# Kernel optimization log

Measured on AMD Instinct MI355X. Metric: run time of the kernel, lower is better.

Reference implementation:

```python
import jax, jax.numpy as jnp
import numpy as np

N_QUBITS = 14
W_MUL = (2.0 ** 0.5) * (5.0 ** -0.5)  # he_std = gain * 5**-0.5, lrmul = 1
TWO_PI = 2.0 * np.pi


def _rx(t):
    c = jnp.cos(t / 2); s = jnp.sin(t / 2)
    return jnp.stack([jnp.stack([c + 0j, -1j * s]), jnp.stack([-1j * s, c + 0j])])


def _ry(t):
    c = jnp.cos(t / 2); s = jnp.sin(t / 2)
    return jnp.stack([jnp.stack([c + 0j, -s + 0j]), jnp.stack([s + 0j, c + 0j])])


def _rz(t):
    e = jnp.exp(-0.5j * t); z = jnp.zeros_like(e)
    return jnp.stack([jnp.stack([e, z]), jnp.stack([z, jnp.conj(e)])])


def _apply_1q(state, gate, q):
    # state: (B,) + (2,)*n ; apply 2x2 gate on qubit q (axis q+1)
    ax = q + 1
    out = jnp.tensordot(gate, state, axes=([1], [ax]))  # new qubit axis at front
    return jnp.moveaxis(out, 0, ax)


_CNOT = jnp.array([[1, 0, 0, 0],
                   [0, 1, 0, 0],
                   [0, 0, 0, 1],
                   [0, 0, 1, 0]], dtype=jnp.complex64).reshape(2, 2, 2, 2)


def _apply_cnot(state, c, t):
    # _CNOT indices: [out_c, out_t, in_c, in_t]
    out = jnp.tensordot(_CNOT, state, axes=([2, 3], [c + 1, t + 1]))
    return jnp.moveaxis(out, (0, 1), (c + 1, t + 1))


def _rot_layer(state, params, gates):
    # per-qubit triple of rotations: params[3*i + j] for gate j on qubit i
    for i in range(N_QUBITS):
        for j, g in enumerate(gates):
            state = _apply_1q(state, g(params[3 * i + j]), i)
    return state


def _ring_of_cnot(state):
    for i in range(N_QUBITS):
        state = _apply_cnot(state, i, (i + 1) % N_QUBITS)
    return state


def _forward(x_real, x_imag, weight):
    n = N_QUBITS
    B = x_real.shape[0]
    psi = (x_real + 1j * x_imag).astype(jnp.complex64).reshape((B,) + (2,) * n)
    w = weight * W_MUL
    layers = [(_rx, _ry, _rz),  # XYZLayer
              (_ry, _rz, _ry),  # YZYLayer
              (_rz, _ry, _rx),  # ZYXLayer
              (_rx, _rz, _rx),  # XZXLayer
              (_ry, _rz, _ry)]  # YZYLayer
    for li, gates in enumerate(layers):
        psi = _rot_layer(psi, w[3 * n * li: 3 * n * (li + 1)], gates)
        if li < len(layers) - 1:
            psi = _ring_of_cnot(psi)
    Z = jnp.array([[1, 0], [0, -1]], dtype=jnp.complex64)
    zpsi = _apply_1q(psi, Z, 0)
    # <psi| Z_0 |psi> (original: conj(psi) row-vector @ (Z_0 psi) column-vector, take real)
    ev = jnp.sum(jnp.conj(psi) * zpsi, axis=tuple(range(1, n + 1))).real
    return ev.reshape(B, 1)  # matches torch (B,1,1).squeeze(-1)


def setup_inputs() -> dict:
    key = jax.random.key(0)
    k1, k2, k3 = jax.random.split(key, 3)
    B = 512
    dim = 2 ** N_QUBITS
    x_real = jax.random.normal(k1, (B, 1, dim), dtype=jnp.float32)
    x_imag = jax.random.normal(k2, (B, 1, dim), dtype=jnp.float32)
    weight = jax.random.uniform(k3, (15 * N_QUBITS,), dtype=jnp.float32) * TWO_PI
    return {"x_real": x_real, "x_imag": x_imag, "weight": weight}


def reference(x_real, x_imag, weight):
    return _forward(x_real, x_imag, weight)
```

## Files before the change

### kernel.cpp

```cpp
#include <hip/hip_runtime.h>
#include <hip/hip_bf16.h>

#define NQ   14
#define DIM  16384
#define BLK  1024
#define WMUL 0.6324555320336759f

typedef float v2f __attribute__((ext_vector_type(2)));

struct C2 { float x, y; };
__device__ inline C2 cmulc(C2 a, C2 b){ return C2{a.x*b.x - a.y*b.y, a.x*b.y + a.y*b.x}; }
__device__ inline C2 caddc(C2 a, C2 b){ return C2{a.x+b.x, a.y+b.y}; }
__device__ inline void mm2(const C2* a, const C2* b, C2* o) {
    o[0] = caddc(cmulc(a[0],b[0]), cmulc(a[1],b[2]));
    o[1] = caddc(cmulc(a[0],b[1]), cmulc(a[1],b[3]));
    o[2] = caddc(cmulc(a[2],b[0]), cmulc(a[3],b[2]));
    o[3] = caddc(cmulc(a[2],b[1]), cmulc(a[3],b[3]));
}
__device__ inline void build_gate(int ty, float t, C2* g) {
    float sn, cs;
    __sincosf(0.5f * t, &sn, &cs);
    if (ty == 0) {
        g[0] = C2{cs, 0.f}; g[1] = C2{0.f, -sn};
        g[2] = C2{0.f, -sn}; g[3] = C2{cs, 0.f};
    } else if (ty == 1) {
        g[0] = C2{cs, 0.f}; g[1] = C2{-sn, 0.f};
        g[2] = C2{sn, 0.f}; g[3] = C2{cs, 0.f};
    } else {
        g[0] = C2{cs, -sn}; g[1] = C2{0.f, 0.f};
        g[2] = C2{0.f, 0.f}; g[3] = C2{cs, sn};
    }
}
__device__ const int TYPES[5][3] = {
    {0,1,2},
    {1,2,1},
    {2,1,0},
    {0,2,0},
    {1,2,1},
};

__global__ void prep_kernel(const float* __restrict__ w, v2f* __restrict__ gg) {
    const int tid = threadIdx.x;
    if (tid < 5 * NQ) {
        const int li = tid / NQ, q = tid % NQ;
        C2 M[4], G[4], T[4];
        #pragma unroll
        for (int j = 0; j < 3; ++j) {
            float t = w[3 * NQ * li + 3 * q + j] * WMUL;
            build_gate(TYPES[li][j], t, G);
            if (j == 0) { M[0]=G[0]; M[1]=G[1]; M[2]=G[2]; M[3]=G[3]; }
            else { mm2(G, M, T); M[0]=T[0]; M[1]=T[1]; M[2]=T[2]; M[3]=T[3]; }
        }
        v2f* gb = &gg[tid * 8];
        #pragma unroll
        for (int k = 0; k < 4; ++k) {
            gb[k * 2 + 0] = v2f{ M[k].x, M[k].x};
            gb[k * 2 + 1] = v2f{-M[k].y, M[k].y};
        }
        if (tid == 4 * NQ + 0) {
            float* mm = (float*)&gg[5 * NQ * 8];
            mm[0] = M[0].x*M[0].x + M[0].y*M[0].y - (M[2].x*M[2].x + M[2].y*M[2].y);
            mm[1] = M[1].x*M[1].x + M[1].y*M[1].y - (M[3].x*M[3].x + M[3].y*M[3].y);
            mm[2] = (M[0].x*M[1].x + M[0].y*M[1].y) - (M[2].x*M[3].x + M[2].y*M[3].y);
            mm[3] = (M[0].x*M[1].y - M[0].y*M[1].x) - (M[2].x*M[3].y - M[2].y*M[3].x);
        }
    }
}

__device__ inline constexpr uint32_t slotf(uint32_t i){
    return i ^ (((i>>4) ^ (i>>8) ^ (i>>12)) & 15u);
}
template<int B> __device__ inline uint32_t ins0(uint32_t t){
    return ((t & ~((1u<<B)-1u)) << 1) | (t & ((1u<<B)-1u));
}
template<int B0,int B1,int B2> __device__ inline uint32_t expand3(uint32_t t){
    return ins0<B2>(ins0<B1>(ins0<B0>(t)));
}
template<int B0,int B1,int B2> __device__ inline constexpr uint32_t rmask3(int r){
    return ((r&1)?(1u<<B0):0u) | ((r&2)?(1u<<B1):0u) | ((r&4)?(1u<<B2):0u);
}

template<int J>
__device__ inline void rot8(v2f* v, const v2f* __restrict__ g){
    const v2f a00=g[0], b00=g[1], a01=g[2], b01=g[3];
    const v2f a10=g[4], b10=g[5], a11=g[6], b11=g[7];
    #pragma unroll
    for (int r = 0; r < 8; ++r){
        if (!(r & (1 << J))) {
            v2f x0 = v[r], x1 = v[r | (1 << J)];
            v2f s0 = x0.yx, s1 = x1.yx;
            v2f y0 = a00*x0 + b00*s0 + a01*x1 + b01*s1;
            v2f y1 = a10*x0 + b10*s0 + a11*x1 + b11*s1;
            v[r] = y0; v[r | (1<<J)] = y1;
        }
    }
}
template<int C, int T>
__device__ inline void cnot8(v2f* v){
    #pragma unroll
    for (int r = 0; r < 8; ++r){
        if ((r & (1 << C)) && !(r & (1 << T))) {
            v2f tt = v[r]; v[r] = v[r | (1 << T)]; v[r | (1 << T)] = tt;
        }
    }
}
template<int T>
__device__ inline void cnotSel(v2f* v, bool c){
    #pragma unroll
    for (int r = 0; r < 8; ++r){
        if (!(r & (1 << T))) {
            v2f lo = v[r], hi = v[r | (1 << T)];
            v[r]          = c ? hi : lo;
            v[r | (1<<T)] = c ? lo : hi;
        }
    }
}

__global__ __launch_bounds__(BLK) void qsim_kernel(
        const float* __restrict__ xr, const float* __restrict__ xi,
        const v2f* __restrict__ gg, float* __restrict__ out) {
    __shared__ v2f s[DIM];
    __shared__ float red[BLK / 64];

    const int b   = blockIdx.x;
    const uint32_t tid = threadIdx.x;

    const float* xrb = xr + (size_t)b * DIM;
    const float* xib = xi + (size_t)b * DIM;

    #define GMP(li, q) (&gg[((li) * NQ + (q)) * 8])

    #define PASS(B0, B1, B2, ...)                                                  \
        _Pragma("unroll 1")                                                        \
        for (uint32_t sl = 0; sl < 2; ++sl) {                                      \
            const uint32_t t  = tid + sl * BLK;                                    \
            const uint32_t sb = slotf(expand3<B0,B1,B2>(t));                       \
            v2f v[8];                                                              \
            _Pragma("unroll")                                                      \
            for (int r = 0; r < 8; ++r)                                            \
                v[r] = s[sb ^ slotf(rmask3<B0,B1,B2>(r))];                         \
            __VA_ARGS__                                                            \
            _Pragma("unroll")                                                      \
            for (int r = 0; r < 8; ++r)                                            \
                s[sb ^ slotf(rmask3<B0,B1,B2>(r))] = v[r];                         \
        }                                                                          \
        __syncthreads();

    float local = 0.f;

    #pragma unroll 1
    for (int li = 0; li < 4; ++li) {
        #pragma unroll 1
        for (uint32_t sl = 0; sl < 2; ++sl) {
            const uint32_t t = tid + sl * BLK;
            v2f v[8];
            if (li == 0) {
                #pragma unroll
                for (int r = 0; r < 8; ++r) {
                    uint32_t i = t | ((uint32_t)r << 11);
                    v[r] = v2f{xrb[i], xib[i]};
                }
            } else {
                const uint32_t sb = slotf(expand3<11,12,13>(t));
                #pragma unroll
                for (int r = 0; r < 8; ++r)
                    v[r] = s[sb ^ slotf(rmask3<11,12,13>(r))];
            }
            rot8<2>(v, GMP(li,0)); rot8<1>(v, GMP(li,1)); rot8<0>(v, GMP(li,2));
            cnot8<2,1>(v); cnot8<1,0>(v);
            const uint32_t sb = slotf(expand3<11,12,13>(t));
            #pragma unroll
            for (int r = 0; r < 8; ++r)
                s[sb ^ slotf(rmask3<11,12,13>(r))] = v[r];
        }
        __syncthreads();

        PASS(8,9,10,
            rot8<2>(v, GMP(li,3)); rot8<1>(v, GMP(li,4)); rot8<0>(v, GMP(li,5));
            cnotSel<2>(v, (t >> 8) & 1u);
            cnot8<2,1>(v); cnot8<1,0>(v);
        )
        PASS(5,6,7,
            rot8<2>(v, GMP(li,6)); rot8<1>(v, GMP(li,7)); rot8<0>(v, GMP(li,8));
            cnotSel<2>(v, (t >> 5) & 1u);
            cnot8<2,1>(v); cnot8<1,0>(v);
        )
        PASS(2,3,4,
            rot8<2>(v, GMP(li,9)); rot8<1>(v, GMP(li,10)); rot8<0>(v, GMP(li,11));
            cnotSel<2>(v, (t >> 2) & 1u);
            cnot8<2,1>(v); cnot8<1,0>(v);
        )
        #pragma unroll 1
        for (uint32_t sl = 0; sl < 2; ++sl) {
            const uint32_t t  = tid + sl * BLK;
            const uint32_t sb = slotf(expand3<0,1,13>(t));
            v2f v[8];
            #pragma unroll
            for (int r = 0; r < 8; ++r)
                v[r] = s[sb ^ slotf(rmask3<0,1,13>(r))];
            rot8<1>(v, GMP(li,12)); rot8<0>(v, GMP(li,13));
            cnotSel<1>(v, t & 1u);
            cnot8<1,0>(v);
            cnot8<0,2>(v);
            if (li < 3) {
                #pragma unroll
                for (int r = 0; r < 8; ++r)
                    s[sb ^ slotf(rmask3<0,1,13>(r))] = v[r];
            } else {
                const float* mm = (const float*)&gg[5 * NQ * 8];
                const float mA = mm[0], mB = mm[1], mP = mm[2], mQ = mm[3];
                #pragma unroll
                for (int r = 0; r < 4; ++r) {
                    v2f a0 = v[r], a1 = v[r | 4];
                    float n0 = a0.x*a0.x + a0.y*a0.y;
                    float n1 = a1.x*a1.x + a1.y*a1.y;
                    float u  = a0.x*a1.x + a0.y*a1.y;
                    float vv = a0.x*a1.y - a0.y*a1.x;
                    local += mA*n0 + mB*n1 + 2.f*(mP*u - mQ*vv);
                }
            }
        }
        if (li < 3) __syncthreads();
    }

    #pragma unroll
    for (int off = 32; off > 0; off >>= 1) local += __shfl_down(local, off);
    const int lane = tid & 63, wid = tid >> 6;
    if (lane == 0) red[wid] = local;
    __syncthreads();
    if (tid == 0) {
        float t = 0.f;
        #pragma unroll
        for (int k = 0; k < BLK / 64; ++k) t += red[k];
        out[b] = t;
    }
}

extern "C" void kernel_launch(void* const* d_in, const int* in_sizes, int n_in,
                              void* d_out, int out_size, void* d_ws, size_t ws_size,
                              hipStream_t stream) {
    const float* xr = (const float*)d_in[0];
    const float* xi = (const float*)d_in[1];
    const float* w  = (const float*)d_in[2];
    float* out = (float*)d_out;
    v2f* gg = (v2f*)d_ws;
    const int B = out_size;
    prep_kernel<<<1, 128, 0, stream>>>(w, gg);
    qsim_kernel<<<B, BLK, 0, stream>>>(xr, xi, gg, out);
}
```

Baseline: 109.6 us.

## Process both slots per thread in split real/imag packed-float layout

Replaces the per-slot sequential loop with a single pass where each thread holds both slots at once. Amplitudes are repacked as separate real and imaginary v2f vectors whose lanes are the two slots, so rotations become packed scalar-broadcast FMAs with no swizzle. Gate coefficients are now stored as plain floats. The intent is to improve packed-FMA use and expose more memory-level parallelism. The cost is doubled register pressure per thread at 1024-thread blocks, plus extra pack and unpack work around each shared-memory access.

```diff
diff --git a/kernel.cpp b/kernel.cpp
--- a/kernel.cpp
+++ b/kernel.cpp
@@ -39,7 +39,7 @@
     {1,2,1},
 };
 
-__global__ void prep_kernel(const float* __restrict__ w, v2f* __restrict__ gg) {
+__global__ void prep_kernel(const float* __restrict__ w, float* __restrict__ gg) {
     const int tid = threadIdx.x;
     if (tid < 5 * NQ) {
         const int li = tid / NQ, q = tid % NQ;
@@ -51,14 +51,11 @@
             if (j == 0) { M[0]=G[0]; M[1]=G[1]; M[2]=G[2]; M[3]=G[3]; }
             else { mm2(G, M, T); M[0]=T[0]; M[1]=T[1]; M[2]=T[2]; M[3]=T[3]; }
         }
-        v2f* gb = &gg[tid * 8];
+        float* gb = &gg[tid * 8];
         #pragma unroll
-        for (int k = 0; k < 4; ++k) {
-            gb[k * 2 + 0] = v2f{ M[k].x, M[k].x};
-            gb[k * 2 + 1] = v2f{-M[k].y, M[k].y};
-        }
+        for (int k = 0; k < 4; ++k) { gb[k*2] = M[k].x; gb[k*2+1] = M[k].y; }
         if (tid == 4 * NQ + 0) {
-            float* mm = (float*)&gg[5 * NQ * 8];
+            float* mm = &gg[5 * NQ * 8];
             mm[0] = M[0].x*M[0].x + M[0].y*M[0].y - (M[2].x*M[2].x + M[2].y*M[2].y);
             mm[1] = M[1].x*M[1].x + M[1].y*M[1].y - (M[3].x*M[3].x + M[3].y*M[3].y);
             mm[2] = (M[0].x*M[1].x + M[0].y*M[1].y) - (M[2].x*M[3].x + M[2].y*M[3].y);
@@ -70,10 +67,10 @@
 __device__ inline constexpr uint32_t slotf(uint32_t i){
     return i ^ (((i>>4) ^ (i>>8) ^ (i>>12)) & 15u);
 }
-template<int B> __device__ inline uint32_t ins0(uint32_t t){
+template<int B> __device__ inline constexpr uint32_t ins0(uint32_t t){
     return ((t & ~((1u<<B)-1u)) << 1) | (t & ((1u<<B)-1u));
 }
-template<int B0,int B1,int B2> __device__ inline uint32_t expand3(uint32_t t){
+template<int B0,int B1,int B2> __device__ inline constexpr uint32_t expand3(uint32_t t){
     return ins0<B2>(ins0<B1>(ins0<B0>(t)));
 }
 template<int B0,int B1,int B2> __device__ inline constexpr uint32_t rmask3(int r){
@@ -81,44 +78,50 @@
 }
 
 template<int J>
-__device__ inline void rot8(v2f* v, const v2f* __restrict__ g){
-    const v2f a00=g[0], b00=g[1], a01=g[2], b01=g[3];
-    const v2f a10=g[4], b10=g[5], a11=g[6], b11=g[7];
+__device__ inline void rotP(v2f* vre, v2f* vim, const float* __restrict__ g){
+    const float are=g[0], aim=g[1], bre=g[2], bim=g[3];
+    const float cre=g[4], cim=g[5], dre=g[6], dim=g[7];
     #pragma unroll
     for (int r = 0; r < 8; ++r){
         if (!(r & (1 << J))) {
-            v2f x0 = v[r], x1 = v[r | (1 << J)];
-            v2f s0 = x0.yx, s1 = x1.yx;
-            v2f y0 = a00*x0 + b00*s0 + a01*x1 + b01*s1;
-            v2f y1 = a10*x0 + b10*s0 + a11*x1 + b11*s1;
-            v[r] = y0; v[r | (1<<J)] = y1;
+            const int r1 = r | (1 << J);
+            v2f x0r = vre[r],  x0i = vim[r];
+            v2f x1r = vre[r1], x1i = vim[r1];
+            vre[r]  = are*x0r - aim*x0i + bre*x1r - bim*x1i;
+            vim[r]  = are*x0i + aim*x0r + bre*x1i + bim*x1r;
+            vre[r1] = cre*x0r - cim*x0i + dre*x1r - dim*x1i;
+            vim[r1] = cre*x0i + cim*x0r + dre*x1i + dim*x1r;
         }
     }
 }
 template<int C, int T>
-__device__ inline void cnot8(v2f* v){
+__device__ inline void cnotP(v2f* vre, v2f* vim){
     #pragma unroll
     for (int r = 0; r < 8; ++r){
         if ((r & (1 << C)) && !(r & (1 << T))) {
-            v2f tt = v[r]; v[r] = v[r | (1 << T)]; v[r | (1 << T)] = tt;
+            const int r1 = r | (1 << T);
+            v2f t0 = vre[r]; vre[r] = vre[r1]; vre[r1] = t0;
+            v2f t1 = vim[r]; vim[r] = vim[r1]; vim[r1] = t1;
         }
     }
 }
 template<int T>
-__device__ inline void cnotSel(v2f* v, bool c){
+__device__ inline void cnotSelP(v2f* vre, v2f* vim, bool c){
     #pragma unroll
     for (int r = 0; r < 8; ++r){
         if (!(r & (1 << T))) {
-            v2f lo = v[r], hi = v[r | (1 << T)];
-            v[r]          = c ? hi : lo;
-            v[r | (1<<T)] = c ? lo : hi;
+            const int r1 = r | (1 << T);
+            v2f lo0 = vre[r], hi0 = vre[r1];
+            v2f lo1 = vim[r], hi1 = vim[r1];
+            vre[r] = c ? hi0 : lo0;  vre[r1] = c ? lo0 : hi0;
+            vim[r] = c ? hi1 : lo1;  vim[r1] = c ? lo1 : hi1;
         }
     }
 }
 
 __global__ __launch_bounds__(BLK) void qsim_kernel(
         const float* __restrict__ xr, const float* __restrict__ xi,
-        const v2f* __restrict__ gg, float* __restrict__ out) {
+        const float* __restrict__ gg, float* __restrict__ out) {
     __shared__ v2f s[DIM];
     __shared__ float red[BLK / 64];
 
@@ -130,19 +133,23 @@
 
     #define GMP(li, q) (&gg[((li) * NQ + (q)) * 8])
 
-    #define PASS(B0, B1, B2, ...)                                                  \
-        _Pragma("unroll 1")                                                        \
-        for (uint32_t sl = 0; sl < 2; ++sl) {                                      \
-            const uint32_t t  = tid + sl * BLK;                                    \
-            const uint32_t sb = slotf(expand3<B0,B1,B2>(t));                       \
-            v2f v[8];                                                              \
+    #define PASS(X0, X1, X2, ...)                                                  \
+        {                                                                          \
+            const uint32_t sbA = slotf(expand3<X0,X1,X2>(tid));                    \
+            const uint32_t sbB = sbA ^ slotf(expand3<X0,X1,X2>((uint32_t)BLK));    \
+            v2f vre[8], vim[8];                                                    \
             _Pragma("unroll")                                                      \
-            for (int r = 0; r < 8; ++r)                                            \
-                v[r] = s[sb ^ slotf(rmask3<B0,B1,B2>(r))];                         \
+            for (int r = 0; r < 8; ++r) {                                          \
+                v2f qa = s[sbA ^ slotf(rmask3<X0,X1,X2>(r))];                      \
+                v2f qb = s[sbB ^ slotf(rmask3<X0,X1,X2>(r))];                      \
+                vre[r] = v2f{qa.x, qb.x}; vim[r] = v2f{qa.y, qb.y};                \
+            }                                                                      \
             __VA_ARGS__                                                            \
             _Pragma("unroll")                                                      \
-            for (int r = 0; r < 8; ++r)                                            \
-                s[sb ^ slotf(rmask3<B0,B1,B2>(r))] = v[r];                         \
+            for (int r = 0; r < 8; ++r) {                                          \
+                s[sbA ^ slotf(rmask3<X0,X1,X2>(r))] = v2f{vre[r].x, vim[r].x};     \
+                s[sbB ^ slotf(rmask3<X0,X1,X2>(r))] = v2f{vre[r].y, vim[r].y};     \
+            }                                                                      \
         }                                                                          \
         __syncthreads();
 
@@ -150,74 +157,96 @@
 
     #pragma unroll 1
     for (int li = 0; li < 4; ++li) {
-        #pragma unroll 1
-        for (uint32_t sl = 0; sl < 2; ++sl) {
-            const uint32_t t = tid + sl * BLK;
-            v2f v[8];
+        {
+            const uint32_t sbA = slotf(expand3<11,12,13>(tid));
+            const uint32_t sbB = sbA ^ slotf(expand3<11,12,13>((uint32_t)BLK));
+            v2f vre[8], vim[8];
             if (li == 0) {
                 #pragma unroll
                 for (int r = 0; r < 8; ++r) {
-                    uint32_t i = t | ((uint32_t)r << 11);
-                    v[r] = v2f{xrb[i], xib[i]};
+                    uint32_t iA = tid | ((uint32_t)r << 11);
+                    uint32_t iB = iA | BLK;
+                    vre[r] = v2f{xrb[iA], xrb[iB]};
+                    vim[r] = v2f{xib[iA], xib[iB]};
                 }
             } else {
-                const uint32_t sb = slotf(expand3<11,12,13>(t));
-                #pragma unroll
-                for (int r = 0; r < 8; ++r)
-                    v[r] = s[sb ^ slotf(rmask3<11,12,13>(r))];
-            }
-            rot8<2>(v, GMP(li,0)); rot8<1>(v, GMP(li,1)); rot8<0>(v, GMP(li,2));
-            cnot8<2,1>(v); cnot8<1,0>(v);
-            const uint32_t sb = slotf(expand3<11,12,13>(t));
+                #pragma unroll
+                for (int r = 0; r < 8; ++r) {
+                    v2f qa = s[sbA ^ slotf(rmask3<11,12,13>(r))];
+                    v2f qb = s[sbB ^ slotf(rmask3<11,12,13>(r))];
+                    vre[r] = v2f{qa.x, qb.x}; vim[r] = v2f{qa.y, qb.y};
+                }
+            }
+            rotP<2>(vre, vim, GMP(li,0));
+            rotP<1>(vre, vim, GMP(li,1));
+            rotP<0>(vre, vim, GMP(li,2));
+            cnotP<2,1>(vre, vim); cnotP<1,0>(vre, vim);
             #pragma unroll
-            for (int r = 0; r < 8; ++r)
-                s[sb ^ slotf(rmask3<11,12,13>(r))] = v[r];
+            for (int r = 0; r < 8; ++r) {
+                s[sbA ^ slotf(rmask3<11,12,13>(r))] = v2f{vre[r].x, vim[r].x};
+                s[sbB ^ slotf(rmask3<11,12,13>(r))] = v2f{vre[r].y, vim[r].y};
+            }
         }
         __syncthreads();
 
         PASS(8,9,10,
-            rot8<2>(v, GMP(li,3)); rot8<1>(v, GMP(li,4)); rot8<0>(v, GMP(li,5));
-            cnotSel<2>(v, (t >> 8) & 1u);
-            cnot8<2,1>(v); cnot8<1,0>(v);
+            rotP<2>(vre, vim, GMP(li,3));
+            rotP<1>(vre, vim, GMP(li,4));
+            rotP<0>(vre, vim, GMP(li,5));
+            cnotSelP<2>(vre, vim, (tid >> 8) & 1u);
+            cnotP<2,1>(vre, vim); cnotP<1,0>(vre, vim);
         )
         PASS(5,6,7,
-            rot8<2>(v, GMP(li,6)); rot8<1>(v, GMP(li,7)); rot8<0>(v, GMP(li,8));
-            cnotSel<2>(v, (t >> 5) & 1u);
-            cnot8<2,1>(v); cnot8<1,0>(v);
+            rotP<2>(vre, vim, GMP(li,6));
+            rotP<1>(vre, vim, GMP(li,7));
+            rotP<0>(vre, vim, GMP(li,8));
+            cnotSelP<2>(vre, vim, (tid >> 5) & 1u);
+            cnotP<2,1>(vre, vim); cnotP<1,0>(vre, vim);
         )
         PASS(2,3,4,
-            rot8<2>(v, GMP(li,9)); rot8<1>(v, GMP(li,10)); rot8<0>(v, GMP(li,11));
-            cnotSel<2>(v, (t >> 2) & 1u);
-            cnot8<2,1>(v); cnot8<1,0>(v);
+            rotP<2>(vre, vim, GMP(li,9));
+            rotP<1>(vre, vim, GMP(li,10));
+            rotP<0>(vre, vim, GMP(li,11));
+            cnotSelP<2>(vre, vim, (tid >> 2) & 1u);
+            cnotP<2,1>(vre, vim); cnotP<1,0>(vre, vim);
         )
-        #pragma unroll 1
-        for (uint32_t sl = 0; sl < 2; ++sl) {
-            const uint32_t t  = tid + sl * BLK;
-            const uint32_t sb = slotf(expand3<0,1,13>(t));
-            v2f v[8];
+        {
+            const uint32_t sbA = slotf(expand3<0,1,13>(tid));
+            const uint32_t sbB = sbA ^ slotf(expand3<0,1,13>((uint32_t)BLK));
+            v2f vre[8], vim[8];
             #pragma unroll
-            for (int r = 0; r < 8; ++r)
-                v[r] = s[sb ^ slotf(rmask3<0,1,13>(r))];
-            rot8<1>(v, GMP(li,12)); rot8<0>(v, GMP(li,13));
-            cnotSel<1>(v, t & 1u);
-            cnot8<1,0>(v);
-            cnot8<0,2>(v);
+            for (int r = 0; r < 8; ++r) {
+                v2f qa = s[sbA ^ slotf(rmask3<0,1,13>(r))];
+                v2f qb = s[sbB ^ slotf(rmask3<0,1,13>(r))];
+                vre[r] = v2f{qa.x, qb.x}; vim[r] = v2f{qa.y, qb.y};
+            }
+            rotP<1>(vre, vim, GMP(li,12));
+            rotP<0>(vre, vim, GMP(li,13));
+            cnotSelP<1>(vre, vim, tid & 1u);
+            cnotP<1,0>(vre, vim);
+            cnotP<0,2>(vre, vim);
             if (li < 3) {
                 #pragma unroll
-                for (int r = 0; r < 8; ++r)
-                    s[sb ^ slotf(rmask3<0,1,13>(r))] = v[r];
+                for (int r = 0; r < 8; ++r) {
+                    s[sbA ^ slotf(rmask3<0,1,13>(r))] = v2f{vre[r].x, vim[r].x};
+                    s[sbB ^ slotf(rmask3<0,1,13>(r))] = v2f{vre[r].y, vim[r].y};
+                }
             } else {
-                const float* mm = (const float*)&gg[5 * NQ * 8];
+                const float* mm = &gg[5 * NQ * 8];
                 const float mA = mm[0], mB = mm[1], mP = mm[2], mQ = mm[3];
+                v2f acc = v2f{0.f, 0.f};
                 #pragma unroll
                 for (int r = 0; r < 4; ++r) {
-                    v2f a0 = v[r], a1 = v[r | 4];
-                    float n0 = a0.x*a0.x + a0.y*a0.y;
-                    float n1 = a1.x*a1.x + a1.y*a1.y;
-                    float u  = a0.x*a1.x + a0.y*a1.y;
-                    float vv = a0.x*a1.y - a0.y*a1.x;
-                    local += mA*n0 + mB*n1 + 2.f*(mP*u - mQ*vv);
-                }
+                    const int r1 = r | 4;
+                    v2f x0r = vre[r],  x0i = vim[r];
+                    v2f x1r = vre[r1], x1i = vim[r1];
+                    v2f n0 = x0r*x0r + x0i*x0i;
+                    v2f n1 = x1r*x1r + x1i*x1i;
+                    v2f u  = x0r*x1r + x0i*x1i;
+                    v2f vv = x0r*x1i - x0i*x1r;
+                    acc += mA*n0 + mB*n1 + 2.f*(mP*u - mQ*vv);
+                }
+                local += acc.x + acc.y;
             }
         }
         if (li < 3) __syncthreads();
@@ -243,7 +272,7 @@
     const float* xi = (const float*)d_in[1];
     const float* w  = (const float*)d_in[2];
     float* out = (float*)d_out;
-    v2f* gg = (v2f*)d_ws;
+    float* gg = (float*)d_ws;
     const int B = out_size;
     prep_kernel<<<1, 128, 0, stream>>>(w, gg);
     qsim_kernel<<<B, BLK, 0, stream>>>(xr, xi, gg, out);
```

Measured after the change: 147.5 us. +34.6%, slower.
